# Kernel tuning notes

Measured on AMD Instinct MI355X. Metric: run time of the kernel, lower is better.

The kernel has to match this reference:

```python
import jax, jax.numpy as jnp
import numpy as np

NEIGHBORS = 16  # init kwarg 'neighbors'


def _mlp(x, params):
    # SetTransform with reduction='none': pointwise MLP, ReLU between layers, linear output
    for W, b in params[:-1]:
        x = jax.nn.relu(x @ W + b)
    W, b = params[-1]
    return x @ W + b


def setup_inputs() -> dict:
    key = jax.random.key(0)
    B, K, P, DIM, C_IN = 4, 2048, 4096, 3, 64
    C_MID, C_OUT = 32, 128
    WH = 32          # weight_hidden sizes
    FH = 256         # final_hidden size
    FIN = C_IN * C_MID  # 2048, final_conv input

    ks = jax.random.split(key, 16)

    def lin(k, fan_in, fan_out):
        k1, k2 = jax.random.split(k)
        s = 1.0 / np.sqrt(fan_in)
        W = jax.random.uniform(k1, (fan_in, fan_out), minval=-s, maxval=s, dtype=jnp.float32)
        b = jax.random.uniform(k2, (fan_out,), minval=-s, maxval=s, dtype=jnp.float32)
        return W, b

    wc0_W, wc0_b = lin(ks[0], DIM, WH)
    wc1_W, wc1_b = lin(ks[1], WH, WH)
    wc2_W, wc2_b = lin(ks[2], WH, C_MID)
    fc0_W, fc0_b = lin(ks[3], FIN, FH)
    fc1_W, fc1_b = lin(ks[4], FH, C_OUT)

    return {
        "keys": jax.random.normal(ks[5], (B, K, DIM), dtype=jnp.float32),
        "points": jax.random.normal(ks[6], (B, P, DIM), dtype=jnp.float32),
        "feats": jax.random.normal(ks[7], (B, P, C_IN), dtype=jnp.float32),
        "wc0_W": wc0_W, "wc0_b": wc0_b,
        "wc1_W": wc1_W, "wc1_b": wc1_b,
        "wc2_W": wc2_W, "wc2_b": wc2_b,
        "fc0_W": fc0_W, "fc0_b": fc0_b,
        "fc1_W": fc1_W, "fc1_b": fc1_b,
    }


def reference(keys, points, feats,
              wc0_W, wc0_b, wc1_W, wc1_b, wc2_W, wc2_b,
              fc0_W, fc0_b, fc1_W, fc1_b):
    B, K, _ = keys.shape
    # Euclidean dist_fn: rel_pos [B,K,P,dim], squared dist [B,K,P]; all points valid
    dist_vec = points[:, None, :, :] - keys[:, :, None, :]
    dist = jnp.sum(dist_vec * dist_vec, axis=-1)
    # k smallest distances -> neighbor indices [B,K,N]
    _, idxs = jax.lax.top_k(-dist, NEIGHBORS)
    # gather relative positions [B,K,N,dim] and neighbor features [B,K,N,c_in]
    neighbor_rel = jnp.take_along_axis(dist_vec, idxs[..., None], axis=2)
    b_idx = jnp.arange(B)[:, None, None]
    neighbor_feats = feats[b_idx, idxs]
    # per-edge weight MLP: [B,K,N,dim] -> [B,K,N,c_mid]
    m = _mlp(neighbor_rel, [(wc0_W, wc0_b), (wc1_W, wc1_b), (wc2_W, wc2_b)])
    # masked matmul aggregation (all neighbors valid under euclidean dist_fn):
    # m^T @ neighbor_feats -> [B,K,c_mid,c_in], flattened to [B,K,c_mid*c_in]
    e = jnp.einsum('bknm,bknc->bkmc', m, neighbor_feats).reshape(B, K, -1)
    # final pointwise MLP -> [B,K,c_out]
    return _mlp(e, [(fc0_W, fc0_b), (fc1_W, fc1_b)])
```

## Files before the change

### kernel.cpp

```cpp
#include <hip/hip_runtime.h>
#include <cfloat>
#include <climits>

#define BATCH 4
#define KQ    2048
#define NP    4096
#define CIN   64
#define CMID  32
#define NB    16
#define NBINS 4096
#define CANDCAP 256
#define QPB   8

typedef short   bf16x8  __attribute__((ext_vector_type(8)));
typedef float   floatx4 __attribute__((ext_vector_type(4)));

__device__ __forceinline__ unsigned short f2bf(float f) {
  unsigned u = __float_as_uint(f);
  u = (u + 0x7fffu + ((u >> 16) & 1u)) >> 16;
  return (unsigned short)u;
}
__device__ __forceinline__ float bf2f(unsigned short u) {
  return __uint_as_float((unsigned)u << 16);
}

__device__ __forceinline__ void load_lds16(const void* g, void* l) {
  __builtin_amdgcn_global_load_lds(
      (const __attribute__((address_space(1))) unsigned int*)g,
      (__attribute__((address_space(3))) unsigned int*)l, 16, 0, 0);
}

__global__ __launch_bounds__(256) void select_topk(
    const float* __restrict__ keys, const float* __restrict__ points,
    int* __restrict__ nidx_g) {
  __shared__ __align__(16) int hist[NBINS];
  __shared__ int   psum[256];
  __shared__ float cand_d[CANDCAP];
  __shared__ int   cand_i[CANDCAP];
  __shared__ int   nidx[NB];
  __shared__ int   sel_cnt, cand_cnt, sBin, sCbelow;

  const int tid = threadIdx.x;
  const int b   = blockIdx.x >> 11;

#pragma unroll
  for (int t = 0; t < 4; ++t)
    *reinterpret_cast<int4*>(&hist[(tid + t * 256) * 4]) = int4{0, 0, 0, 0};
  if (tid == 0) { sel_cnt = 0; cand_cnt = 0; }

  const float kx = keys[blockIdx.x * 3 + 0];
  const float ky = keys[blockIdx.x * 3 + 1];
  const float kz = keys[blockIdx.x * 3 + 2];
  __syncthreads();

  const float4* pv =
      reinterpret_cast<const float4*>(points + (size_t)b * NP * 3) + (size_t)tid * 12;
  float f[48];
#pragma unroll
  for (int c = 0; c < 12; ++c) {
    const float4 v = pv[c];
    f[c * 4 + 0] = v.x; f[c * 4 + 1] = v.y; f[c * 4 + 2] = v.z; f[c * 4 + 3] = v.w;
  }
  float dreg[16];
#pragma unroll
  for (int j = 0; j < 16; ++j) {
    const float dx = f[j * 3 + 0] - kx;
    const float dy = f[j * 3 + 1] - ky;
    const float dz = f[j * 3 + 2] - kz;
    const float d  = dx * dx + dy * dy + dz * dz;
    dreg[j] = d;
    atomicAdd(&hist[__float_as_uint(d) >> 19], 1);
  }
  __syncthreads();

  {
    const int base = tid * 16;
    int s = 0;
#pragma unroll
    for (int t = 0; t < 4; ++t) {
      const int4 hv = *reinterpret_cast<const int4*>(&hist[base + t * 4]);
      s += hv.x + hv.y + hv.z + hv.w;
    }
    psum[tid] = s;
  }
  __syncthreads();

  if (tid < 64) {
    const int q = psum[tid * 4] + psum[tid * 4 + 1] + psum[tid * 4 + 2] + psum[tid * 4 + 3];
    int incl = q;
#pragma unroll
    for (int off = 1; off < 64; off <<= 1) {
      int u = __shfl_up(incl, off);
      if (tid >= off) incl += u;
    }
    unsigned long long bal = __ballot(incl >= NB);
    int firstlane = __ffsll((long long)bal) - 1;
    if (tid == firstlane) {
      int cum = incl - q;
      int bin = -1;
      for (int t = 0; t < 4 && bin < 0; ++t) {
        const int ps = psum[tid * 4 + t];
        if (cum + ps >= NB) {
          const int b0 = (tid * 4 + t) * 16;
          for (int j = 0; j < 16; ++j) {
            const int h = hist[b0 + j];
            if (cum + h >= NB) { bin = b0 + j; break; }
            cum += h;
          }
        } else cum += ps;
      }
      sBin = bin; sCbelow = cum;
    }
  }
  __syncthreads();

  const unsigned B = (unsigned)sBin;
#pragma unroll
  for (int j = 0; j < 16; ++j) {
    const int i = tid * 16 + j;
    const unsigned bk = __float_as_uint(dreg[j]) >> 19;
    if (bk < B) {
      int pos = atomicAdd(&sel_cnt, 1);
      nidx[pos] = i;
    } else if (bk == B) {
      int pos = atomicAdd(&cand_cnt, 1);
      if (pos < CANDCAP) { cand_d[pos] = dreg[j]; cand_i[pos] = i; }
    }
  }
  __syncthreads();

  if (tid < 64) {
    const int rem = NB - sCbelow;
    const int cc  = min(cand_cnt, CANDCAP);
    for (int s = 0; s < rem; ++s) {
      float bd = FLT_MAX; int bi = INT_MAX; int bp = -1;
      for (int j = tid; j < cc; j += 64) {
        float d = cand_d[j]; int ii = cand_i[j];
        if (d < bd || (d == bd && ii < bi)) { bd = d; bi = ii; bp = j; }
      }
#pragma unroll
      for (int off = 32; off > 0; off >>= 1) {
        float od = __shfl_down(bd, off);
        int   oi = __shfl_down(bi, off);
        int   op = __shfl_down(bp, off);
        if (od < bd || (od == bd && oi < bi)) { bd = od; bi = oi; bp = op; }
      }
      if (tid == 0) { nidx[sCbelow + s] = bi; cand_d[bp] = FLT_MAX; }
    }
  }
  __syncthreads();

  if (tid < NB) nidx_g[blockIdx.x * NB + tid] = nidx[tid];
}

__global__ __launch_bounds__(256) void edge_prep(
    const float* __restrict__ keys, const float* __restrict__ points,
    const float* __restrict__ feats, const int* __restrict__ nidx_g,
    const float* __restrict__ wc0_W, const float* __restrict__ wc0_b,
    const float* __restrict__ wc1_W, const float* __restrict__ wc1_b,
    const float* __restrict__ wc2_W, const float* __restrict__ wc2_b,
    const float* __restrict__ fc0_W, const float* __restrict__ fc1_W,
    unsigned short* __restrict__ W0T, unsigned short* __restrict__ W1T,
    unsigned short* __restrict__ E) {
  __shared__ __align__(16) float w0[96], b0v[32], w1[1024], b1v[32], w2[1024], b2v[32];
  __shared__ int   idx_s[QPB * NB];
  __shared__ __align__(16) unsigned short m_bf[QPB * NB][40];
  __shared__ __align__(16) char u_mem[128 * 144];
  float (*h2_all)[36]        = reinterpret_cast<float(*)[36]>(u_mem);
  unsigned short (*f_bf)[72] = reinterpret_cast<unsigned short(*)[72]>(u_mem);
  float (*tt)[33]            = reinterpret_cast<float(*)[33]>(u_mem);

  const int tid = threadIdx.x;
  const int bid = blockIdx.x;
  const int q0  = bid * QPB;
  const int b   = q0 >> 11;

  if (bid < 544) {
    const float* W; unsigned short* WT; int K, N, k0, n0;
    if (bid < 512) { W = fc0_W; WT = W0T; K = 2048; N = 256;
                     k0 = (bid >> 3) * 32; n0 = (bid & 7) * 32; }
    else           { W = fc1_W; WT = W1T; K = 256;  N = 128;
                     k0 = ((bid - 512) >> 2) * 32; n0 = ((bid - 512) & 3) * 32; }
    const int tx = tid & 31, ty = tid >> 5;
#pragma unroll
    for (int p = 0; p < 4; ++p)
      tt[ty + p * 8][tx] = W[(size_t)(k0 + ty + p * 8) * N + n0 + tx];
    __syncthreads();
#pragma unroll
    for (int p = 0; p < 4; ++p)
      WT[(size_t)(n0 + ty + p * 8) * K + k0 + tx] = f2bf(tt[tx][ty + p * 8]);
    __syncthreads();
  }

  if (tid < 96) w0[tid] = wc0_W[tid];
  for (int i = tid; i < 1024; i += 256) { w1[i] = wc1_W[i]; w2[i] = wc2_W[i]; }
  if (tid < 32) { b0v[tid] = wc0_b[tid]; b1v[tid] = wc1_b[tid]; b2v[tid] = wc2_b[tid]; }
  if (tid < QPB * NB) idx_s[tid] = nidx_g[q0 * NB + tid];
  __syncthreads();

  const int edge = tid & 127;
  const int half = tid >> 7;
  const int ob   = half * 16;
  const int qe   = edge >> 4;
  const int idx  = idx_s[edge];
  {
    const float* p  = points + ((size_t)b * NP + idx) * 3;
    const float* kq = keys + (size_t)(q0 + qe) * 3;
    const float rx = p[0] - kq[0], ry = p[1] - kq[1], rz = p[2] - kq[2];

    float h1[32];
#pragma unroll
    for (int o4 = 0; o4 < 8; ++o4) {
      const float4 a = *reinterpret_cast<const float4*>(&w0[o4 * 4]);
      const float4 c = *reinterpret_cast<const float4*>(&w0[32 + o4 * 4]);
      const float4 d = *reinterpret_cast<const float4*>(&w0[64 + o4 * 4]);
      const float4 e = *reinterpret_cast<const float4*>(&b0v[o4 * 4]);
      h1[o4 * 4 + 0] = fmaxf(0.f, rx * a.x + ry * c.x + rz * d.x + e.x);
      h1[o4 * 4 + 1] = fmaxf(0.f, rx * a.y + ry * c.y + rz * d.y + e.y);
      h1[o4 * 4 + 2] = fmaxf(0.f, rx * a.z + ry * c.z + rz * d.z + e.z);
      h1[o4 * 4 + 3] = fmaxf(0.f, rx * a.w + ry * c.w + rz * d.w + e.w);
    }

    float acc2[16];
#pragma unroll
    for (int j = 0; j < 16; ++j) acc2[j] = b1v[ob + j];
#pragma unroll
    for (int i = 0; i < 32; ++i) {
      const float hv = h1[i];
#pragma unroll
      for (int j4 = 0; j4 < 4; ++j4) {
        const float4 w = *reinterpret_cast<const float4*>(&w1[i * 32 + ob + j4 * 4]);
        acc2[j4 * 4 + 0] += hv * w.x;
        acc2[j4 * 4 + 1] += hv * w.y;
        acc2[j4 * 4 + 2] += hv * w.z;
        acc2[j4 * 4 + 3] += hv * w.w;
      }
    }
#pragma unroll
    for (int j4 = 0; j4 < 4; ++j4) {
      float4 o4v;
      o4v.x = fmaxf(acc2[j4 * 4 + 0], 0.f);
      o4v.y = fmaxf(acc2[j4 * 4 + 1], 0.f);
      o4v.z = fmaxf(acc2[j4 * 4 + 2], 0.f);
      o4v.w = fmaxf(acc2[j4 * 4 + 3], 0.f);
      *reinterpret_cast<float4*>(&h2_all[edge][ob + j4 * 4]) = o4v;
    }
  }
  __syncthreads();

  float mo[16];
#pragma unroll
  for (int j = 0; j < 16; ++j) mo[j] = b2v[ob + j];
#pragma unroll
  for (int i = 0; i < 32; ++i) {
    const float hv = h2_all[edge][i];
#pragma unroll
    for (int j4 = 0; j4 < 4; ++j4) {
      const float4 w = *reinterpret_cast<const float4*>(&w2[i * 32 + ob + j4 * 4]);
      mo[j4 * 4 + 0] += hv * w.x;
      mo[j4 * 4 + 1] += hv * w.y;
      mo[j4 * 4 + 2] += hv * w.z;
      mo[j4 * 4 + 3] += hv * w.w;
    }
  }
#pragma unroll
  for (int j = 0; j < 8; ++j) {
    const unsigned lo = f2bf(mo[2 * j]), hi = f2bf(mo[2 * j + 1]);
    *reinterpret_cast<unsigned*>(&m_bf[edge][ob + 2 * j]) = lo | (hi << 16);
  }
  __syncthreads();

#pragma unroll
  for (int t = 0; t < 8; ++t) {
    const int task = tid + t * 256;
    const int row = task >> 4, ch = task & 15;
    const float4 v = *reinterpret_cast<const float4*>(
        feats + ((size_t)b * NP + idx_s[row]) * CIN + ch * 4);
    ushort4 o4;
    o4.x = f2bf(v.x); o4.y = f2bf(v.y); o4.z = f2bf(v.z); o4.w = f2bf(v.w);
    *reinterpret_cast<ushort4*>(&f_bf[row][ch * 4]) = o4;
  }
  __syncthreads();

  const int wv = tid >> 6, lane = tid & 63;
  const int co = lane & 7, mg = lane >> 3;
#pragma unroll
  for (int it = 0; it < 2; ++it) {
    const int q = wv + it * 4;
    float acc[4][8] = {};
#pragma unroll
    for (int n = 0; n < 16; ++n) {
      const int row = q * 16 + n;
      const ushort4 m4 = *reinterpret_cast<const ushort4*>(&m_bf[row][mg * 4]);
      const float mv[4] = {bf2f(m4.x), bf2f(m4.y), bf2f(m4.z), bf2f(m4.w)};
      const uint4 fv = *reinterpret_cast<const uint4*>(&f_bf[row][co * 8]);
      float fc[8];
      fc[0] = __uint_as_float(fv.x << 16); fc[1] = __uint_as_float(fv.x & 0xffff0000u);
      fc[2] = __uint_as_float(fv.y << 16); fc[3] = __uint_as_float(fv.y & 0xffff0000u);
      fc[4] = __uint_as_float(fv.z << 16); fc[5] = __uint_as_float(fv.z & 0xffff0000u);
      fc[6] = __uint_as_float(fv.w << 16); fc[7] = __uint_as_float(fv.w & 0xffff0000u);
#pragma unroll
      for (int i = 0; i < 4; ++i)
#pragma unroll
        for (int j = 0; j < 8; ++j) acc[i][j] += mv[i] * fc[j];
    }
    unsigned short* Eq = E + (size_t)(q0 + q) * 2048;
#pragma unroll
    for (int i = 0; i < 4; ++i) {
      const int mid = mg * 4 + i;
      uint4 o;
      o.x = (unsigned)f2bf(acc[i][0]) | ((unsigned)f2bf(acc[i][1]) << 16);
      o.y = (unsigned)f2bf(acc[i][2]) | ((unsigned)f2bf(acc[i][3]) << 16);
      o.z = (unsigned)f2bf(acc[i][4]) | ((unsigned)f2bf(acc[i][5]) << 16);
      o.w = (unsigned)f2bf(acc[i][6]) | ((unsigned)f2bf(acc[i][7]) << 16);
      *reinterpret_cast<uint4*>(&Eq[mid * 64 + co * 8]) = o;
    }
  }
}

template <int KDIM, bool RELU, bool OUTBF16>
__global__ __launch_bounds__(256) void gemm_mfma(
    const unsigned short* __restrict__ A,
    const unsigned short* __restrict__ Bt,
    const float* __restrict__ bias,
    void* __restrict__ Cout, int ldc) {
  __shared__ __align__(16) unsigned short Al[64 * 128];
  __shared__ __align__(16) unsigned short Bl[64 * 128];
  const int tid  = threadIdx.x;
  const int m0   = blockIdx.x * 64, n0 = blockIdx.y * 64;
  const int wv   = tid >> 6, lane = tid & 63;
  const int quad = lane >> 4, s = lane & 15;
  const int moff = (wv & 1) * 32, noff = (wv >> 1) * 32;
  const int lr   = lane >> 4;
  const int lc   = lane & 15;

  floatx4 acc[2][2] = {{{0.f,0.f,0.f,0.f},{0.f,0.f,0.f,0.f}},
                       {{0.f,0.f,0.f,0.f},{0.f,0.f,0.f,0.f}}};

  for (int k0 = 0; k0 < KDIM; k0 += 128) {
#pragma unroll
    for (int t = 0; t < 4; ++t) {
      const int R0 = wv * 16 + t * 4;
      const int r  = R0 + lr;
      const int gc = lc ^ (r & 7);
      load_lds16(A  + (size_t)(m0 + r) * KDIM + k0 + gc * 8, &Al[R0 * 128]);
      load_lds16(Bt + (size_t)(n0 + r) * KDIM + k0 + gc * 8, &Bl[R0 * 128]);
    }
    __syncthreads();
#pragma unroll
    for (int h = 0; h < 4; ++h) {
      bf16x8 af[2], bfr[2];
#pragma unroll
      for (int i = 0; i < 2; ++i) {
        const int r = moff + i * 16 + s;
        af[i] = *reinterpret_cast<const bf16x8*>(
            &Al[(size_t)r * 128 + ((((h << 2) | quad) ^ (r & 7)) << 3)]);
      }
#pragma unroll
      for (int j = 0; j < 2; ++j) {
        const int r = noff + j * 16 + s;
        bfr[j] = *reinterpret_cast<const bf16x8*>(
            &Bl[(size_t)r * 128 + ((((h << 2) | quad) ^ (r & 7)) << 3)]);
      }
#pragma unroll
      for (int i = 0; i < 2; ++i)
#pragma unroll
        for (int j = 0; j < 2; ++j)
          acc[i][j] = __builtin_amdgcn_mfma_f32_16x16x32_bf16(af[i], bfr[j], acc[i][j], 0, 0, 0);
    }
    __syncthreads();
  }

#pragma unroll
  for (int i = 0; i < 2; ++i)
#pragma unroll
    for (int j = 0; j < 2; ++j) {
      const int col = n0 + noff + j * 16 + s;
      const float bv = bias[col];
#pragma unroll
      for (int r = 0; r < 4; ++r) {
        const int row = m0 + moff + i * 16 + quad * 4 + r;
        float v = acc[i][j][r] + bv;
        if (RELU) v = fmaxf(v, 0.f);
        if (OUTBF16)
          ((unsigned short*)Cout)[(size_t)row * ldc + col] = f2bf(v);
        else
          ((float*)Cout)[(size_t)row * ldc + col] = v;
      }
    }
}

extern "C" void kernel_launch(void* const* d_in, const int* in_sizes, int n_in,
                              void* d_out, int out_size, void* d_ws, size_t ws_size,
                              hipStream_t stream) {
  const float* keys   = (const float*)d_in[0];
  const float* points = (const float*)d_in[1];
  const float* feats  = (const float*)d_in[2];
  const float* wc0_W  = (const float*)d_in[3];
  const float* wc0_b  = (const float*)d_in[4];
  const float* wc1_W  = (const float*)d_in[5];
  const float* wc1_b  = (const float*)d_in[6];
  const float* wc2_W  = (const float*)d_in[7];
  const float* wc2_b  = (const float*)d_in[8];
  const float* fc0_W  = (const float*)d_in[9];
  const float* fc0_b  = (const float*)d_in[10];
  const float* fc1_W  = (const float*)d_in[11];
  const float* fc1_b  = (const float*)d_in[12];
  float* out = (float*)d_out;

  const int M = BATCH * KQ;
  char* ws = (char*)d_ws;
  unsigned short* E    = (unsigned short*)(ws);
  unsigned short* H16  = (unsigned short*)(ws + (size_t)33554432);
  unsigned short* W0T  = (unsigned short*)(ws + (size_t)37748736);
  unsigned short* W1T  = (unsigned short*)(ws + (size_t)38797312);
  int*            nidx = (int*)(ws + (size_t)38862848);

  select_topk<<<M, 256, 0, stream>>>(keys, points, nidx);
  edge_prep<<<M / QPB, 256, 0, stream>>>(keys, points, feats, nidx,
                                         wc0_W, wc0_b, wc1_W, wc1_b, wc2_W, wc2_b,
                                         fc0_W, fc1_W, W0T, W1T, E);
  gemm_mfma<2048, true,  true ><<<dim3(M / 64, 4), 256, 0, stream>>>(E, W0T, fc0_b, H16, 256);
  gemm_mfma<256,  false, false><<<dim3(M / 64, 2), 256, 0, stream>>>(H16, W1T, fc1_b, out, 128);
}
```

Before: 168.6 us.

## Rank-based parallel candidate selection and XCD-aware block swizzle for first GEMM

Replaces the serial per-step argmin loop (one wavefront, rem iterations of a shuffle reduction) in top-k candidate selection with a parallel rank computation, where each of the 256 threads computes the rank of its candidate and scatters it directly. This removes the dependent reduction chain, at the cost of O(cc^2) shared-memory reads. It also remaps block indices in the first GEMM so that blocks landing on the same XCD (L&7) share M rows across the four N tiles, aiming to improve L2 reuse of the A operand.

New measurement: 170.7 us. Within noise of the previous version (+1.3%).

```diff
diff --git a/kernel.cpp b/kernel.cpp
--- a/kernel.cpp
+++ b/kernel.cpp
@@ -129,23 +129,17 @@
   }
   __syncthreads();
 
-  if (tid < 64) {
+  {
     const int rem = NB - sCbelow;
     const int cc  = min(cand_cnt, CANDCAP);
-    for (int s = 0; s < rem; ++s) {
-      float bd = FLT_MAX; int bi = INT_MAX; int bp = -1;
-      for (int j = tid; j < cc; j += 64) {
-        float d = cand_d[j]; int ii = cand_i[j];
-        if (d < bd || (d == bd && ii < bi)) { bd = d; bi = ii; bp = j; }
-      }
-#pragma unroll
-      for (int off = 32; off > 0; off >>= 1) {
-        float od = __shfl_down(bd, off);
-        int   oi = __shfl_down(bi, off);
-        int   op = __shfl_down(bp, off);
-        if (od < bd || (od == bd && oi < bi)) { bd = od; bi = oi; bp = op; }
-      }
-      if (tid == 0) { nidx[sCbelow + s] = bi; cand_d[bp] = FLT_MAX; }
+    for (int j = tid; j < cc; j += 256) {
+      const float dj = cand_d[j]; const int ij = cand_i[j];
+      int rank = 0;
+      for (int k = 0; k < cc; ++k) {
+        const float dk = cand_d[k]; const int ik = cand_i[k];
+        rank += (dk < dj || (dk == dj && ik < ij)) ? 1 : 0;
+      }
+      if (rank < rem) nidx[sCbelow + rank] = ij;
     }
   }
   __syncthreads();
@@ -318,7 +312,7 @@
   }
 }
 
-template <int KDIM, bool RELU, bool OUTBF16>
+template <int KDIM, bool RELU, bool OUTBF16, bool SWIZZLE>
 __global__ __launch_bounds__(256) void gemm_mfma(
     const unsigned short* __restrict__ A,
     const unsigned short* __restrict__ Bt,
@@ -327,7 +321,16 @@
   __shared__ __align__(16) unsigned short Al[64 * 128];
   __shared__ __align__(16) unsigned short Bl[64 * 128];
   const int tid  = threadIdx.x;
-  const int m0   = blockIdx.x * 64, n0 = blockIdx.y * 64;
+  int m0, n0;
+  if (SWIZZLE) {
+    const int L    = blockIdx.x;
+    const int slot = L >> 3;
+    m0 = ((L & 7) * 16 + (slot >> 2)) * 64;
+    n0 = (slot & 3) * 64;
+  } else {
+    m0 = blockIdx.x * 64;
+    n0 = blockIdx.y * 64;
+  }
   const int wv   = tid >> 6, lane = tid & 63;
   const int quad = lane >> 4, s = lane & 15;
   const int moff = (wv & 1) * 32, noff = (wv >> 1) * 32;
@@ -420,6 +423,6 @@
   edge_prep<<<M / QPB, 256, 0, stream>>>(keys, points, feats, nidx,
                                          wc0_W, wc0_b, wc1_W, wc1_b, wc2_W, wc2_b,
                                          fc0_W, fc1_W, W0T, W1T, E);
-  gemm_mfma<2048, true,  true ><<<dim3(M / 64, 4), 256, 0, stream>>>(E, W0T, fc0_b, H16, 256);
-  gemm_mfma<256,  false, false><<<dim3(M / 64, 2), 256, 0, stream>>>(H16, W1T, fc1_b, out, 128);
-}
+  gemm_mfma<2048, true,  true,  true ><<<512, 256, 0, stream>>>(E, W0T, fc0_b, H16, 256);
+  gemm_mfma<256,  false, false, false><<<dim3(M / 64, 2), 256, 0, stream>>>(H16, W1T, fc1_b, out, 128);
+}
```
